# Optimization experiments

Measured on AMD Instinct MI355X. Metric: run time of the kernel, lower is better.

The kernel has to match this reference:

```python
import jax, jax.numpy as jnp
import numpy as np

EPS = 1e-5  # BatchNorm eps


def _spmm(x, src, dst, dinv, n):
    # normalized adjacency SpMM: out[d] = dinv[d] * sum_{(s,d) in E} dinv[s] * x[s]
    msg = x[src] * dinv[src][:, None]                      # [E, d]
    agg = jax.ops.segment_sum(msg, dst, num_segments=n)   # [N, d]
    return agg * dinv[:, None]


def _cheb(x, W, b, src, dst, dinv, n):
    # Chebyshev recursion with lambda_max=2: Lhat = -Ahat
    # T0 = X, T1 = Lhat X, Tk = 2 Lhat T_{k-1} - T_{k-2}; out = sum_k T_k W_k + b
    X0 = x
    X1 = -_spmm(x, src, dst, dinv, n)
    out = X0 @ W[0] + X1 @ W[1]
    Xp, Xc = X0, X1
    for k in range(2, W.shape[0]):
        Xn = -2.0 * _spmm(Xc, src, dst, dinv, n) - Xp
        out = out + Xn @ W[k]
        Xp, Xc = Xc, Xn
    return out + b


def _bn(x, gamma, beta):
    # BatchNorm1d over nodes (training-mode batch stats)
    mu = jnp.mean(x, axis=0)
    var = jnp.var(x, axis=0)
    return (x - mu) * jax.lax.rsqrt(var + EPS) * gamma + beta


def setup_inputs() -> dict:
    key = jax.random.key(0)
    ks = jax.random.split(key, 8)
    n, e, fin, h, fout, K = 50000, 800000, 128, 128, 64, 3
    def w(k, shape, fan_in):
        return jax.random.normal(k, shape, jnp.float32) * np.float32(1.0 / np.sqrt(fan_in))
    return {
        "features": jax.random.normal(ks[0], (n, fin), jnp.float32),
        "src": jax.random.randint(ks[1], (e,), 0, n),
        "dst": jax.random.randint(ks[2], (e,), 0, n),
        "W1": w(ks[3], (K, fin, h), K * fin), "b1": jnp.zeros((h,), jnp.float32),
        "W2": w(ks[4], (K, h, h), K * h), "b2": jnp.zeros((h,), jnp.float32),
        "W3": w(ks[5], (K, h, h), K * h), "b3": jnp.zeros((h,), jnp.float32),
        "gamma": jnp.ones((h,), jnp.float32), "beta": jnp.zeros((h,), jnp.float32),
        "mw1": w(ks[6], (h, h), h), "mb1": jnp.zeros((h,), jnp.float32),
        "mw2": w(ks[7], (h, fout), h), "mb2": jnp.zeros((fout,), jnp.float32),
    }


def reference(features, src, dst, W1, b1, W2, b2, W3, b3, gamma, beta, mw1, mb1, mw2, mb2):
    n = features.shape[0]
    deg = jax.ops.segment_sum(jnp.ones(dst.shape, features.dtype), dst, num_segments=n)
    dinv = jax.lax.rsqrt(jnp.maximum(deg, 1.0))
    x = jax.nn.relu(_cheb(features, W1, b1, src, dst, dinv, n))
    x = _bn(x, gamma, beta)
    for _ in range(1, 3):  # self.k = 3 -> cheb2 applied twice (shared weights)
        x = jax.nn.relu(_cheb(x, W2, b2, src, dst, dinv, n))
    x_res = x
    x = jax.nn.relu(_cheb(x, W3, b3, src, dst, dinv, n))
    x = x + x_res  # dropout treated as identity (eval mode)
    return jax.nn.relu(x @ mw1 + mb1) @ mw2 + mb2
```

## Files before the change

kernel.cpp:

```cpp
#include <hip/hip_runtime.h>
#include <hip/hip_bf16.h>

typedef __attribute__((ext_vector_type(4))) float f32x4;
typedef __attribute__((ext_vector_type(8))) short short8;

__device__ inline unsigned short f2bf(float f) {
    union { float f; unsigned int u; } v; v.f = f;
    unsigned int u = v.u;
    return (unsigned short)((u + 0x7fffu + ((u >> 16) & 1u)) >> 16);
}
__device__ inline float bf2f(unsigned short h) {
    union { unsigned int u; float f; } v; v.u = ((unsigned int)h) << 16; return v.f;
}
__device__ inline float bflo(unsigned int p) {
    union { unsigned int u; float f; } v; v.u = p << 16; return v.f;
}
__device__ inline float bfhi(unsigned int p) {
    union { unsigned int u; float f; } v; v.u = p & 0xffff0000u; return v.f;
}
__device__ inline unsigned int packbf(float a, float b) {
    return (unsigned int)f2bf(a) | ((unsigned int)f2bf(b) << 16);
}

#define EPT 4096


__global__ __launch_bounds__(256) void cast_k(const float* __restrict__ x, unsigned short* __restrict__ y, int n4) {
    int i = blockIdx.x * 256 + threadIdx.x;
    if (i >= n4) return;
    f32x4 v = ((const f32x4*)x)[i];
    uint2 o; o.x = packbf(v[0], v[1]); o.y = packbf(v[2], v[3]);
    ((uint2*)y)[i] = o;
}


__global__ __launch_bounds__(256) void deg_count8_k(const int* __restrict__ dst, int* __restrict__ deg,
                                                    int e, int n, int n8) {
    int r = blockIdx.x & 7;
    int chunk = blockIdx.x >> 3;
    int base = chunk * EPT;
    int lim = base + EPT; if (lim > e) lim = e;
    int lo = r * n8;
    int hi = lo + n8; if (hi > n) hi = n;
    for (int i = base + threadIdx.x; i < lim; i += 256) {
        int d = dst[i];
        if (d >= lo && d < hi) atomicAdd(&deg[d], 1);
    }
}

__global__ __launch_bounds__(256) void partial_k(const int* __restrict__ deg, int* __restrict__ part, int n) {
    __shared__ int sm[256];
    int t = threadIdx.x;
    int base = blockIdx.x * 1024 + t * 4;
    int s = 0;
#pragma unroll
    for (int j = 0; j < 4; ++j) { int idx = base + j; if (idx < n) s += deg[idx]; }
    sm[t] = s;
    __syncthreads();
    for (int off = 128; off > 0; off >>= 1) {
        if (t < off) sm[t] += sm[t + off];
        __syncthreads();
    }
    if (t == 0) part[blockIdx.x] = sm[0];
}

__global__ __launch_bounds__(256) void scanpart_k(int* __restrict__ part, int nb) {
    __shared__ int sm[256];
    int t = threadIdx.x;
    int v = (t < nb) ? part[t] : 0;
    sm[t] = v;
    __syncthreads();
    for (int off = 1; off < 256; off <<= 1) {
        int u = (t >= off) ? sm[t - off] : 0;
        __syncthreads();
        sm[t] += u;
        __syncthreads();
    }
    if (t < nb) part[t] = sm[t] - v;
}

__global__ __launch_bounds__(256) void rowptr_k(const int* __restrict__ deg, const int* __restrict__ part,
                                                int* __restrict__ rowptr, int* __restrict__ cursor,
                                                float* __restrict__ dinv, int n) {
    __shared__ int sm[256];
    int t = threadIdx.x;
    int base = blockIdx.x * 1024 + t * 4;
    int d[4]; int s = 0;
#pragma unroll
    for (int j = 0; j < 4; ++j) { int idx = base + j; d[j] = (idx < n) ? deg[idx] : 0; s += d[j]; }
    sm[t] = s;
    __syncthreads();
    for (int off = 1; off < 256; off <<= 1) {
        int u = (t >= off) ? sm[t - off] : 0;
        __syncthreads();
        sm[t] += u;
        __syncthreads();
    }
    int ex = part[blockIdx.x] + sm[t] - s;
#pragma unroll
    for (int j = 0; j < 4; ++j) {
        int idx = base + j;
        if (idx < n) {
            rowptr[idx] = ex; cursor[idx] = ex;
            dinv[idx] = rsqrtf(fmaxf((float)d[j], 1.0f));
        }
        ex += d[j];
    }
    if (blockIdx.x == gridDim.x - 1 && t == 255) rowptr[n] = part[blockIdx.x] + sm[255];
}

__global__ __launch_bounds__(256) void scatter8_k(const int* __restrict__ src, const int* __restrict__ dst,
                                                  int* __restrict__ cursor, int* __restrict__ csrc,
                                                  int e, int n, int n8) {
    int r = blockIdx.x & 7;
    int chunk = blockIdx.x >> 3;
    int base = chunk * EPT;
    int lim = base + EPT; if (lim > e) lim = e;
    int lo = r * n8;
    int hi = lo + n8; if (hi > n) hi = n;
    for (int i = base + threadIdx.x; i < lim; i += 256) {
        int d = dst[i];
        if (d >= lo && d < hi) {
            int p = atomicAdd(&cursor[d], 1);
            csrc[p] = src[i];
        }
    }
}


template<bool AFF>
__global__ __launch_bounds__(256) void spmm_bf_k(const unsigned short* __restrict__ x, const int* __restrict__ rowptr,
                                                 const int* __restrict__ csrc, const float* __restrict__ dinv,
                                                 const float* __restrict__ gscale, const float* __restrict__ goff,
                                                 unsigned short* __restrict__ out, int n) {
    int lane = threadIdx.x & 63;
    int wave = threadIdx.x >> 6;
    int node = blockIdx.x * 4 + wave;
    if (node >= n) return;
    int g = lane >> 4;
    int c = lane & 15;
    int beg = rowptr[node], end = rowptr[node + 1];
    float acc[8];
    float sw = 0.f;
#pragma unroll
    for (int j = 0; j < 8; ++j) acc[j] = 0.f;

    int i = beg + g;
    for (; i + 12 < end; i += 16) {
        int s0 = csrc[i], s1 = csrc[i + 4], s2 = csrc[i + 8], s3 = csrc[i + 12];
        float w0 = dinv[s0], w1 = dinv[s1], w2 = dinv[s2], w3 = dinv[s3];
        uint4 v0 = ((const uint4*)(x + (size_t)s0 * 128))[c];
        uint4 v1 = ((const uint4*)(x + (size_t)s1 * 128))[c];
        uint4 v2 = ((const uint4*)(x + (size_t)s2 * 128))[c];
        uint4 v3 = ((const uint4*)(x + (size_t)s3 * 128))[c];
        if (AFF) sw += w0 + w1 + w2 + w3;
        acc[0] += w0 * bflo(v0.x); acc[1] += w0 * bfhi(v0.x);
        acc[2] += w0 * bflo(v0.y); acc[3] += w0 * bfhi(v0.y);
        acc[4] += w0 * bflo(v0.z); acc[5] += w0 * bfhi(v0.z);
        acc[6] += w0 * bflo(v0.w); acc[7] += w0 * bfhi(v0.w);
        acc[0] += w1 * bflo(v1.x); acc[1] += w1 * bfhi(v1.x);
        acc[2] += w1 * bflo(v1.y); acc[3] += w1 * bfhi(v1.y);
        acc[4] += w1 * bflo(v1.z); acc[5] += w1 * bfhi(v1.z);
        acc[6] += w1 * bflo(v1.w); acc[7] += w1 * bfhi(v1.w);
        acc[0] += w2 * bflo(v2.x); acc[1] += w2 * bfhi(v2.x);
        acc[2] += w2 * bflo(v2.y); acc[3] += w2 * bfhi(v2.y);
        acc[4] += w2 * bflo(v2.z); acc[5] += w2 * bfhi(v2.z);
        acc[6] += w2 * bflo(v2.w); acc[7] += w2 * bfhi(v2.w);
        acc[0] += w3 * bflo(v3.x); acc[1] += w3 * bfhi(v3.x);
        acc[2] += w3 * bflo(v3.y); acc[3] += w3 * bfhi(v3.y);
        acc[4] += w3 * bflo(v3.z); acc[5] += w3 * bfhi(v3.z);
        acc[6] += w3 * bflo(v3.w); acc[7] += w3 * bfhi(v3.w);
    }
    for (; i < end; i += 4) {
        int s0 = csrc[i];
        float w0 = dinv[s0];
        uint4 v0 = ((const uint4*)(x + (size_t)s0 * 128))[c];
        if (AFF) sw += w0;
        acc[0] += w0 * bflo(v0.x); acc[1] += w0 * bfhi(v0.x);
        acc[2] += w0 * bflo(v0.y); acc[3] += w0 * bfhi(v0.y);
        acc[4] += w0 * bflo(v0.z); acc[5] += w0 * bfhi(v0.z);
        acc[6] += w0 * bflo(v0.w); acc[7] += w0 * bfhi(v0.w);
    }

#pragma unroll
    for (int j = 0; j < 8; ++j) {
        acc[j] += __shfl_xor(acc[j], 16, 64);
        acc[j] += __shfl_xor(acc[j], 32, 64);
    }
    if (AFF) {
        sw += __shfl_xor(sw, 16, 64);
        sw += __shfl_xor(sw, 32, 64);
    }

    float dd = dinv[node];
    if (g == 0) {
        if (AFF) {
            f32x4 sc0 = ((const f32x4*)(gscale + c * 8))[0];
            f32x4 sc1 = ((const f32x4*)(gscale + c * 8))[1];
            f32x4 of0 = ((const f32x4*)(goff + c * 8))[0];
            f32x4 of1 = ((const f32x4*)(goff + c * 8))[1];
#pragma unroll
            for (int j = 0; j < 4; ++j) {
                acc[j] = sc0[j] * acc[j] + of0[j] * sw;
                acc[4 + j] = sc1[j] * acc[4 + j] + of1[j] * sw;
            }
        }
        uint4 o;
        o.x = packbf(acc[0] * dd, acc[1] * dd);
        o.y = packbf(acc[2] * dd, acc[3] * dd);
        o.z = packbf(acc[4] * dd, acc[5] * dd);
        o.w = packbf(acc[6] * dd, acc[7] * dd);
        ((uint4*)(out + (size_t)node * 128))[c] = o;
    }
}


__device__ inline void pack_one(const float* __restrict__ W, unsigned short* __restrict__ out,
                                int K, int N, int cheb, int id) {
    int total = (K / 32) * (N / 16) * 64;
    if (id >= total) return;
    int lane = id & 63;
    int t2 = id >> 6;
    int nf = N / 16;
    int f = t2 % nf;
    int ks = t2 / nf;
    int col = f * 16 + (lane & 15);
    int kbase = ks * 32 + ((lane >> 4) * 8);
    for (int j = 0; j < 8; ++j) {
        int kg = kbase + j;
        float v;
        if (cheb) {
            int t = kg >> 7, kk = kg & 127;
            float w0 = W[kk * 128 + col], wb = W[16384 + kk * 128 + col], wc = W[32768 + kk * 128 + col];
            v = (t == 0) ? (w0 - wc) : (t == 1) ? (-wb) : (2.0f * wc);
        } else {
            v = W[(size_t)kg * N + col];
        }
        out[(size_t)id * 8 + j] = f2bf(v);
    }
}

__global__ __launch_bounds__(256) void pack_all_k(const float* W1, unsigned short* wp1,
                                                  const float* W2, unsigned short* wp2,
                                                  const float* W3, unsigned short* wp3,
                                                  const float* mw1, unsigned short* wpm1,
                                                  const float* mw2, unsigned short* wpm2) {
    int b = blockIdx.x, t = threadIdx.x;
    if (b < 24)       pack_one(W1, wp1, 384, 128, 1, b * 256 + t);
    else if (b < 48)  pack_one(W2, wp2, 384, 128, 1, (b - 24) * 256 + t);
    else if (b < 72)  pack_one(W3, wp3, 384, 128, 1, (b - 48) * 256 + t);
    else if (b < 80)  pack_one(mw1, wpm1, 128, 128, 0, (b - 72) * 256 + t);
    else              pack_one(mw2, wpm2, 128, 64, 0, (b - 80) * 256 + t);
}


__global__ __launch_bounds__(128) void bn_coef_k(const float* __restrict__ gsum, const float* __restrict__ gsqs,
                                                 const float* __restrict__ gamma, const float* __restrict__ beta,
                                                 float* __restrict__ gscale, float* __restrict__ goff, float inv_n) {
    int c = threadIdx.x;
    float mu = gsum[c] * inv_n;
    float var = gsqs[c] * inv_n - mu * mu;
    float sc = rsqrtf(var + 1e-5f) * gamma[c];
    gscale[c] = sc;
    goff[c] = beta[c] - mu * sc;
}


template<bool RELU, bool RES, bool STATS, bool AFFA>
__global__ __launch_bounds__(256, 3) void gemm_k(const unsigned short* __restrict__ s0,
                                                 const unsigned short* __restrict__ s1,
                                                 const unsigned short* __restrict__ s2,
                                                 const unsigned short* __restrict__ wp,
                                                 const float* __restrict__ bias,
                                                 const unsigned short* __restrict__ resid,
                                                 const float* __restrict__ gscale,
                                                 const float* __restrict__ goff,
                                                 float* __restrict__ gsum, float* __restrict__ gsqs,
                                                 unsigned short* __restrict__ outp, int n) {
    __shared__ char blds[49152];
    __shared__ float bs[128], bq[128];
    int t = threadIdx.x;
    int lane = t & 63;
    int wave = t >> 6;
    int row0 = blockIdx.x * 64;

    if (STATS && t < 128) { bs[t] = 0.f; bq[t] = 0.f; }

    int rowA = row0 + wave * 16 + (lane & 15);
    if (rowA >= n) rowA = n - 1;
    int kg = (lane >> 4) * 8;

    {
        const char* gsrc = (const char*)wp;
        int wbase = wave * 12288;
#pragma unroll
        for (int j = 0; j < 12; ++j) {
            int off = wbase + j * 1024;
            __builtin_amdgcn_global_load_lds((const unsigned int*)(gsrc + off + lane * 16),
                                             (unsigned int*)(blds + off), 16, 0, 0);
        }
    }

    short8 a[12];
#pragma unroll
    for (int ks = 0; ks < 12; ++ks) {
        const unsigned short* sp = (ks < 4) ? s0 : ((ks < 8) ? s1 : s2);
        int kk = (ks & 3) * 32 + kg;
        a[ks] = *(const short8*)(sp + (size_t)rowA * 128 + kk);
    }
    if (AFFA) {
#pragma unroll
        for (int ks = 0; ks < 4; ++ks) {
            int kk = ks * 32 + kg;
            union { unsigned short u[8]; short8 v; } af;
#pragma unroll
            for (int j = 0; j < 8; ++j) {
                float xv = bf2f((unsigned short)a[ks][j]);
                af.u[j] = f2bf(xv * gscale[kk + j] + goff[kk + j]);
            }
            a[ks] = af.v;
        }
    }

    f32x4 acc[8];
#pragma unroll
    for (int f = 0; f < 8; ++f) acc[f] = (f32x4)(0.0f);

#pragma unroll
    for (int half = 0; half < 2; ++half) {
        __syncthreads();

#pragma unroll
        for (int ks6 = 0; ks6 < 6; ++ks6) {
            int ks = half * 6 + ks6;
#pragma unroll
            for (int f = 0; f < 8; ++f) {
                short8 bb = *(const short8*)(blds + (ks6 * 8 + f) * 1024 + lane * 16);
                acc[f] = __builtin_amdgcn_mfma_f32_16x16x32_bf16(a[ks], bb, acc[f], 0, 0, 0);
            }
        }

        if (half == 0) {
            __syncthreads();
            const char* gsrc = (const char*)wp + 49152;
            int wbase = wave * 12288;
#pragma unroll
            for (int j = 0; j < 12; ++j) {
                int off = wbase + j * 1024;
                __builtin_amdgcn_global_load_lds((const unsigned int*)(gsrc + off + lane * 16),
                                                 (unsigned int*)(blds + off), 16, 0, 0);
            }
        }
    }

    int colb = lane & 15;
    int rowD = row0 + wave * 16 + ((lane >> 4) << 2);
#pragma unroll
    for (int f = 0; f < 8; ++f) {
        int c = f * 16 + colb;
        float bv = bias[c];
        float ls = 0.f, lq = 0.f;
#pragma unroll
        for (int r = 0; r < 4; ++r) {
            int row = rowD + r;
            if (row >= n) continue;
            float v = acc[f][r] + bv;
            if (RELU) v = fmaxf(v, 0.0f);
            if (RES) v += bf2f(resid[(size_t)row * 128 + c]);
            if (STATS) { ls += v; lq += v * v; }
            outp[(size_t)row * 128 + c] = f2bf(v);
        }
        if (STATS) { atomicAdd(&bs[c], ls); atomicAdd(&bq[c], lq); }
    }

    if (STATS) {
        __syncthreads();
        if (t < 128) {
            atomicAdd(&gsum[t], bs[t]);
            atomicAdd(&gsqs[t], bq[t]);
        }
    }
}


__global__ __launch_bounds__(256, 3) void mlp_fused_k(const unsigned short* __restrict__ x,
                                                      const unsigned short* __restrict__ wpm1,
                                                      const float* __restrict__ mb1,
                                                      const unsigned short* __restrict__ wpm2,
                                                      const float* __restrict__ mb2,
                                                      float* __restrict__ out, int n) {
    __shared__ char alds[49152];
    int t = threadIdx.x;
    int lane = t & 63;
    int wave = t >> 6;
    int row0 = blockIdx.x * 64 + wave * 16;
    int rowA = row0 + (lane & 15);
    if (rowA >= n) rowA = n - 1;
    int kg = (lane >> 4) * 8;
    int colb = lane & 15;

    {
        int wbase = wave * 12288;
#pragma unroll
        for (int j = 0; j < 12; ++j) {
            int off = wbase + j * 1024;
            const char* g = (off < 32768) ? ((const char*)wpm1 + off)
                                          : ((const char*)wpm2 + (off - 32768));
            __builtin_amdgcn_global_load_lds((const unsigned int*)(g + lane * 16),
                                             (unsigned int*)(alds + off), 16, 0, 0);
        }
    }

    short8 a[4];
#pragma unroll
    for (int ks = 0; ks < 4; ++ks)
        a[ks] = *(const short8*)(x + (size_t)rowA * 128 + ks * 32 + kg);

    __syncthreads();

    f32x4 acc[8];
#pragma unroll
    for (int f = 0; f < 8; ++f) acc[f] = (f32x4)(0.0f);
#pragma unroll
    for (int ks = 0; ks < 4; ++ks) {
#pragma unroll
        for (int f = 0; f < 8; ++f) {
            short8 b = *(const short8*)(alds + (ks * 8 + f) * 1024 + lane * 16);
            acc[f] = __builtin_amdgcn_mfma_f32_16x16x32_bf16(a[ks], b, acc[f], 0, 0, 0);
        }
    }
    __syncthreads();

    int lrowD = wave * 16 + ((lane >> 4) << 2);
#pragma unroll
    for (int f = 0; f < 8; ++f) {
        int c = f * 16 + colb;
        float bv = mb1[c];
#pragma unroll
        for (int r = 0; r < 4; ++r) {
            int lrow = lrowD + r;
            float v = fmaxf(acc[f][r] + bv, 0.0f);
            int byte = lrow * 256 + c * 2;
            byte ^= ((lrow & 7) << 4);
            *(unsigned short*)(alds + byte) = f2bf(v);
        }
    }
    __syncthreads();

    f32x4 acc2[4];
#pragma unroll
    for (int f = 0; f < 4; ++f) acc2[f] = (f32x4)(0.0f);
    int lrowA = wave * 16 + (lane & 15);
#pragma unroll
    for (int ks = 0; ks < 4; ++ks) {
        int byte = lrowA * 256 + (ks * 32 + kg) * 2;
        byte ^= ((lrowA & 7) << 4);
        short8 av = *(const short8*)(alds + byte);
#pragma unroll
        for (int f = 0; f < 4; ++f) {
            short8 b = *(const short8*)(alds + 32768 + (ks * 4 + f) * 1024 + lane * 16);
            acc2[f] = __builtin_amdgcn_mfma_f32_16x16x32_bf16(av, b, acc2[f], 0, 0, 0);
        }
    }
    int rowD = row0 + ((lane >> 4) << 2);
#pragma unroll
    for (int f = 0; f < 4; ++f) {
        int c = f * 16 + colb;
        float bv = mb2[c];
#pragma unroll
        for (int r = 0; r < 4; ++r) {
            int row = rowD + r;
            if (row >= n) continue;
            out[(size_t)row * 64 + c] = acc2[f][r] + bv;
        }
    }
}


extern "C" void kernel_launch(void* const* d_in, const int* in_sizes, int n_in,
                              void* d_out, int out_size, void* d_ws, size_t ws_size,
                              hipStream_t stream) {
    const float* feat  = (const float*)d_in[0];
    const int*   src   = (const int*)d_in[1];
    const int*   dst   = (const int*)d_in[2];
    const float* W1    = (const float*)d_in[3];
    const float* b1    = (const float*)d_in[4];
    const float* W2    = (const float*)d_in[5];
    const float* b2    = (const float*)d_in[6];
    const float* W3    = (const float*)d_in[7];
    const float* b3    = (const float*)d_in[8];
    const float* gamma = (const float*)d_in[9];
    const float* beta  = (const float*)d_in[10];
    const float* mw1   = (const float*)d_in[11];
    const float* mb1   = (const float*)d_in[12];
    const float* mw2   = (const float*)d_in[13];
    const float* mb2   = (const float*)d_in[14];
    float* outp = (float*)d_out;

    const int n = in_sizes[0] / 128;
    const int e = in_sizes[1];
    const int n8 = (n + 7) / 8;

    char* w = (char*)d_ws;
    auto alloc = [&](size_t bytes) -> void* {
        void* p = (void*)w;
        w += (bytes + 255) & ~(size_t)255;
        return p;
    };
    unsigned short* featb = (unsigned short*)alloc((size_t)n * 128 * 2);
    unsigned short* buf0  = (unsigned short*)alloc((size_t)n * 128 * 2);
    unsigned short* buf1  = (unsigned short*)alloc((size_t)n * 128 * 2);
    unsigned short* buf2  = (unsigned short*)alloc((size_t)n * 128 * 2);
    unsigned short* buf3  = (unsigned short*)alloc((size_t)n * 128 * 2);
    int*   deg    = (int*)alloc((size_t)n * 4);
    float* dinv   = (float*)alloc((size_t)n * 4);
    int*   rowptr = (int*)alloc((size_t)(n + 1) * 4);
    int*   cursor = (int*)alloc((size_t)n * 4);
    int*   csrc   = (int*)alloc((size_t)e * 4);
    int*   part   = (int*)alloc(256 * 4);
    unsigned short* wp1  = (unsigned short*)alloc(12 * 8 * 512 * 2);
    unsigned short* wp2  = (unsigned short*)alloc(12 * 8 * 512 * 2);
    unsigned short* wp3  = (unsigned short*)alloc(12 * 8 * 512 * 2);
    unsigned short* wpm1 = (unsigned short*)alloc(4 * 8 * 512 * 2);
    unsigned short* wpm2 = (unsigned short*)alloc(4 * 4 * 512 * 2);
    float* gsum   = (float*)alloc(128 * 4);
    float* gsqs   = (float*)alloc(128 * 4);
    float* gscale = (float*)alloc(128 * 4);
    float* goff   = (float*)alloc(128 * 4);

    const int gGemm = (n + 63) / 64;
    const int gSpmm = (n + 3) / 4;
    const int nb = (n + 1023) / 1024;
    const int gE8 = 8 * ((e + EPT - 1) / EPT);

    cast_k<<<(n * 32 + 255) / 256, 256, 0, stream>>>(feat, featb, n * 32);
    hipMemsetAsync(deg, 0, (size_t)n * 4, stream);
    hipMemsetAsync(gsum, 0, 1024, stream);
    deg_count8_k<<<gE8, 256, 0, stream>>>(dst, deg, e, n, n8);
    partial_k<<<nb, 256, 0, stream>>>(deg, part, n);
    scanpart_k<<<1, 256, 0, stream>>>(part, nb);
    rowptr_k<<<nb, 256, 0, stream>>>(deg, part, rowptr, cursor, dinv, n);
    scatter8_k<<<gE8, 256, 0, stream>>>(src, dst, cursor, csrc, e, n, n8);
    pack_all_k<<<84, 256, 0, stream>>>(W1, wp1, W2, wp2, W3, wp3, mw1, wpm1, mw2, wpm2);

    spmm_bf_k<false><<<gSpmm, 256, 0, stream>>>(featb, rowptr, csrc, dinv, nullptr, nullptr, buf1, n);
    spmm_bf_k<false><<<gSpmm, 256, 0, stream>>>(buf1, rowptr, csrc, dinv, nullptr, nullptr, buf2, n);
    gemm_k<true, false, true, false><<<gGemm, 256, 0, stream>>>(
        featb, buf1, buf2, wp1, b1, nullptr, nullptr, nullptr, gsum, gsqs, buf0, n);
    bn_coef_k<<<1, 128, 0, stream>>>(gsum, gsqs, gamma, beta, gscale, goff, 1.0f / (float)n);

    spmm_bf_k<true><<<gSpmm, 256, 0, stream>>>(buf0, rowptr, csrc, dinv, gscale, goff, buf1, n);
    spmm_bf_k<false><<<gSpmm, 256, 0, stream>>>(buf1, rowptr, csrc, dinv, nullptr, nullptr, buf2, n);
    gemm_k<true, false, false, true><<<gGemm, 256, 0, stream>>>(
        buf0, buf1, buf2, wp2, b2, nullptr, gscale, goff, nullptr, nullptr, buf3, n);

    spmm_bf_k<false><<<gSpmm, 256, 0, stream>>>(buf3, rowptr, csrc, dinv, nullptr, nullptr, buf1, n);
    spmm_bf_k<false><<<gSpmm, 256, 0, stream>>>(buf1, rowptr, csrc, dinv, nullptr, nullptr, buf2, n);
    gemm_k<true, false, false, false><<<gGemm, 256, 0, stream>>>(
        buf3, buf1, buf2, wp2, b2, nullptr, nullptr, nullptr, nullptr, nullptr, buf0, n);

    spmm_bf_k<false><<<gSpmm, 256, 0, stream>>>(buf0, rowptr, csrc, dinv, nullptr, nullptr, buf1, n);
    spmm_bf_k<false><<<gSpmm, 256, 0, stream>>>(buf1, rowptr, csrc, dinv, nullptr, nullptr, buf2, n);
    gemm_k<true, true, false, false><<<gGemm, 256, 0, stream>>>(
        buf0, buf1, buf2, wp3, b3, buf0, nullptr, nullptr, nullptr, nullptr, buf3, n);

    mlp_fused_k<<<gGemm, 256, 0, stream>>>(buf3, wpm1, mb1, wpm2, mb2, outp, n);
}
```

Measured before the change: 482.3 us.

## Fuse MLP head into final Chebyshev GEMM and use 512-thread 128-row blocks

The final Chebyshev GEMM now keeps its 128-row output tile in swizzled LDS and runs both MLP layers in place, so the separate MLP kernel and its global round trip of the hidden activations go away. All GEMM launches also move to 512-thread blocks covering 128 rows, so each block loads the packed weights into LDS once for twice as many rows. An empty asm barrier pins the A fragments in registers. The risks are higher LDS use per block (an extra 32KB in the MLP variant) and register pressure under launch_bounds(512,4).

```diff
diff --git a/kernel.cpp b/kernel.cpp
--- a/kernel.cpp
+++ b/kernel.cpp
@@ -266,8 +266,8 @@
 }
 
 
-template<bool RELU, bool RES, bool STATS, bool AFFA>
-__global__ __launch_bounds__(256, 3) void gemm_k(const unsigned short* __restrict__ s0,
+template<bool RELU, bool RES, bool STATS, bool AFFA, bool MLP>
+__global__ __launch_bounds__(512, 4) void gemm_k(const unsigned short* __restrict__ s0,
                                                  const unsigned short* __restrict__ s1,
                                                  const unsigned short* __restrict__ s2,
                                                  const unsigned short* __restrict__ wp,
@@ -276,25 +276,32 @@
                                                  const float* __restrict__ gscale,
                                                  const float* __restrict__ goff,
                                                  float* __restrict__ gsum, float* __restrict__ gsqs,
-                                                 unsigned short* __restrict__ outp, int n) {
+                                                 unsigned short* __restrict__ outp,
+                                                 const unsigned short* __restrict__ wpm1,
+                                                 const float* __restrict__ mb1,
+                                                 const unsigned short* __restrict__ wpm2,
+                                                 const float* __restrict__ mb2,
+                                                 float* __restrict__ outf, int n) {
     __shared__ char blds[49152];
-    __shared__ float bs[128], bq[128];
+    __shared__ char tl[MLP ? 32768 : 16];
+    __shared__ float bs[STATS ? 128 : 1], bq[STATS ? 128 : 1];
     int t = threadIdx.x;
     int lane = t & 63;
     int wave = t >> 6;
-    int row0 = blockIdx.x * 64;
+    int row0 = blockIdx.x * 128;
 
     if (STATS && t < 128) { bs[t] = 0.f; bq[t] = 0.f; }
 
     int rowA = row0 + wave * 16 + (lane & 15);
     if (rowA >= n) rowA = n - 1;
     int kg = (lane >> 4) * 8;
+    int colb = lane & 15;
 
     {
         const char* gsrc = (const char*)wp;
-        int wbase = wave * 12288;
-#pragma unroll
-        for (int j = 0; j < 12; ++j) {
+        int wbase = wave * 6144;
+#pragma unroll
+        for (int j = 0; j < 6; ++j) {
             int off = wbase + j * 1024;
             __builtin_amdgcn_global_load_lds((const unsigned int*)(gsrc + off + lane * 16),
                                              (unsigned int*)(blds + off), 16, 0, 0);
@@ -321,6 +328,11 @@
             a[ks] = af.v;
         }
     }
+#pragma unroll
+    for (int ks = 0; ks < 12; ++ks) {
+        f32x4 kv = *(f32x4*)&a[ks];
+        asm volatile("" :: "v"(kv));
+    }
 
     f32x4 acc[8];
 #pragma unroll
@@ -343,9 +355,9 @@
         if (half == 0) {
             __syncthreads();
             const char* gsrc = (const char*)wp + 49152;
-            int wbase = wave * 12288;
-#pragma unroll
-            for (int j = 0; j < 12; ++j) {
+            int wbase = wave * 6144;
+#pragma unroll
+            for (int j = 0; j < 6; ++j) {
                 int off = wbase + j * 1024;
                 __builtin_amdgcn_global_load_lds((const unsigned int*)(gsrc + off + lane * 16),
                                                  (unsigned int*)(blds + off), 16, 0, 0);
@@ -353,8 +365,8 @@
         }
     }
 
-    int colb = lane & 15;
     int rowD = row0 + wave * 16 + ((lane >> 4) << 2);
+    int lrowD = wave * 16 + ((lane >> 4) << 2);
 #pragma unroll
     for (int f = 0; f < 8; ++f) {
         int c = f * 16 + colb;
@@ -368,7 +380,14 @@
             if (RELU) v = fmaxf(v, 0.0f);
             if (RES) v += bf2f(resid[(size_t)row * 128 + c]);
             if (STATS) { ls += v; lq += v * v; }
-            outp[(size_t)row * 128 + c] = f2bf(v);
+            if (MLP) {
+                int lrow = lrowD + r;
+                int byte = lrow * 256 + c * 2;
+                byte ^= ((lrow & 7) << 4);
+                *(unsigned short*)(tl + byte) = f2bf(v);
+            } else {
+                outp[(size_t)row * 128 + c] = f2bf(v);
+            }
         }
         if (STATS) { atomicAdd(&bs[c], ls); atomicAdd(&bq[c], lq); }
     }
@@ -380,98 +399,78 @@
             atomicAdd(&gsqs[t], bq[t]);
         }
     }
-}
-
-
-__global__ __launch_bounds__(256, 3) void mlp_fused_k(const unsigned short* __restrict__ x,
-                                                      const unsigned short* __restrict__ wpm1,
-                                                      const float* __restrict__ mb1,
-                                                      const unsigned short* __restrict__ wpm2,
-                                                      const float* __restrict__ mb2,
-                                                      float* __restrict__ out, int n) {
-    __shared__ char alds[49152];
-    int t = threadIdx.x;
-    int lane = t & 63;
-    int wave = t >> 6;
-    int row0 = blockIdx.x * 64 + wave * 16;
-    int rowA = row0 + (lane & 15);
-    if (rowA >= n) rowA = n - 1;
-    int kg = (lane >> 4) * 8;
-    int colb = lane & 15;
-
-    {
-        int wbase = wave * 12288;
-#pragma unroll
-        for (int j = 0; j < 12; ++j) {
-            int off = wbase + j * 1024;
-            const char* g = (off < 32768) ? ((const char*)wpm1 + off)
-                                          : ((const char*)wpm2 + (off - 32768));
-            __builtin_amdgcn_global_load_lds((const unsigned int*)(g + lane * 16),
-                                             (unsigned int*)(alds + off), 16, 0, 0);
-        }
-    }
-
-    short8 a[4];
-#pragma unroll
-    for (int ks = 0; ks < 4; ++ks)
-        a[ks] = *(const short8*)(x + (size_t)rowA * 128 + ks * 32 + kg);
-
-    __syncthreads();
-
-    f32x4 acc[8];
-#pragma unroll
-    for (int f = 0; f < 8; ++f) acc[f] = (f32x4)(0.0f);
-#pragma unroll
-    for (int ks = 0; ks < 4; ++ks) {
+
+    if (MLP) {
+        __syncthreads();
+        {
+            int wbase = wave * 6144;
+#pragma unroll
+            for (int j = 0; j < 6; ++j) {
+                int off = wbase + j * 1024;
+                const char* g = (off < 32768) ? ((const char*)wpm1 + off)
+                                              : ((const char*)wpm2 + (off - 32768));
+                __builtin_amdgcn_global_load_lds((const unsigned int*)(g + lane * 16),
+                                                 (unsigned int*)(blds + off), 16, 0, 0);
+            }
+        }
+        __syncthreads();
+
+        int lrowA = wave * 16 + (lane & 15);
+        f32x4 acc2[8];
+#pragma unroll
+        for (int f = 0; f < 8; ++f) acc2[f] = (f32x4)(0.0f);
+#pragma unroll
+        for (int ks = 0; ks < 4; ++ks) {
+            int byte = lrowA * 256 + (ks * 32 + kg) * 2;
+            byte ^= ((lrowA & 7) << 4);
+            short8 av = *(const short8*)(tl + byte);
+#pragma unroll
+            for (int f = 0; f < 8; ++f) {
+                short8 b = *(const short8*)(blds + (ks * 8 + f) * 1024 + lane * 16);
+                acc2[f] = __builtin_amdgcn_mfma_f32_16x16x32_bf16(av, b, acc2[f], 0, 0, 0);
+            }
+        }
+        __syncthreads();
+
 #pragma unroll
         for (int f = 0; f < 8; ++f) {
-            short8 b = *(const short8*)(alds + (ks * 8 + f) * 1024 + lane * 16);
-            acc[f] = __builtin_amdgcn_mfma_f32_16x16x32_bf16(a[ks], b, acc[f], 0, 0, 0);
-        }
-    }
-    __syncthreads();
-
-    int lrowD = wave * 16 + ((lane >> 4) << 2);
-#pragma unroll
-    for (int f = 0; f < 8; ++f) {
-        int c = f * 16 + colb;
-        float bv = mb1[c];
-#pragma unroll
-        for (int r = 0; r < 4; ++r) {
-            int lrow = lrowD + r;
-            float v = fmaxf(acc[f][r] + bv, 0.0f);
-            int byte = lrow * 256 + c * 2;
-            byte ^= ((lrow & 7) << 4);
-            *(unsigned short*)(alds + byte) = f2bf(v);
-        }
-    }
-    __syncthreads();
-
-    f32x4 acc2[4];
-#pragma unroll
-    for (int f = 0; f < 4; ++f) acc2[f] = (f32x4)(0.0f);
-    int lrowA = wave * 16 + (lane & 15);
-#pragma unroll
-    for (int ks = 0; ks < 4; ++ks) {
-        int byte = lrowA * 256 + (ks * 32 + kg) * 2;
-        byte ^= ((lrowA & 7) << 4);
-        short8 av = *(const short8*)(alds + byte);
+            int c = f * 16 + colb;
+            float bv = mb1[c];
+#pragma unroll
+            for (int r = 0; r < 4; ++r) {
+                int lrow = lrowD + r;
+                float v = fmaxf(acc2[f][r] + bv, 0.0f);
+                int byte = lrow * 256 + c * 2;
+                byte ^= ((lrow & 7) << 4);
+                *(unsigned short*)(tl + byte) = f2bf(v);
+            }
+        }
+        __syncthreads();
+
+        f32x4 acc3[4];
+#pragma unroll
+        for (int f = 0; f < 4; ++f) acc3[f] = (f32x4)(0.0f);
+#pragma unroll
+        for (int ks = 0; ks < 4; ++ks) {
+            int byte = lrowA * 256 + (ks * 32 + kg) * 2;
+            byte ^= ((lrowA & 7) << 4);
+            short8 av = *(const short8*)(tl + byte);
+#pragma unroll
+            for (int f = 0; f < 4; ++f) {
+                short8 b = *(const short8*)(blds + 32768 + (ks * 4 + f) * 1024 + lane * 16);
+                acc3[f] = __builtin_amdgcn_mfma_f32_16x16x32_bf16(av, b, acc3[f], 0, 0, 0);
+            }
+        }
 #pragma unroll
         for (int f = 0; f < 4; ++f) {
-            short8 b = *(const short8*)(alds + 32768 + (ks * 4 + f) * 1024 + lane * 16);
-            acc2[f] = __builtin_amdgcn_mfma_f32_16x16x32_bf16(av, b, acc2[f], 0, 0, 0);
-        }
-    }
-    int rowD = row0 + ((lane >> 4) << 2);
-#pragma unroll
-    for (int f = 0; f < 4; ++f) {
-        int c = f * 16 + colb;
-        float bv = mb2[c];
-#pragma unroll
-        for (int r = 0; r < 4; ++r) {
-            int row = rowD + r;
-            if (row >= n) continue;
-            out[(size_t)row * 64 + c] = acc2[f][r] + bv;
+            int c = f * 16 + colb;
+            float bv = mb2[c];
+#pragma unroll
+            for (int r = 0; r < 4; ++r) {
+                int row = rowD + r;
+                if (row >= n) continue;
+                outf[(size_t)row * 64 + c] = acc3[f][r] + bv;
+            }
         }
     }
 }
@@ -528,7 +527,7 @@
     float* gscale = (float*)alloc(128 * 4);
     float* goff   = (float*)alloc(128 * 4);
 
-    const int gGemm = (n + 63) / 64;
+    const int gGemm = (n + 127) / 128;
     const int gSpmm = (n + 3) / 4;
     const int nb = (n + 1023) / 1024;
     const int gE8 = 8 * ((e + EPT - 1) / EPT);
@@ -545,24 +544,26 @@
 
     spmm_bf_k<false><<<gSpmm, 256, 0, stream>>>(featb, rowptr, csrc, dinv, nullptr, nullptr, buf1, n);
     spmm_bf_k<false><<<gSpmm, 256, 0, stream>>>(buf1, rowptr, csrc, dinv, nullptr, nullptr, buf2, n);
-    gemm_k<true, false, true, false><<<gGemm, 256, 0, stream>>>(
-        featb, buf1, buf2, wp1, b1, nullptr, nullptr, nullptr, gsum, gsqs, buf0, n);
+    gemm_k<true, false, true, false, false><<<gGemm, 512, 0, stream>>>(
+        featb, buf1, buf2, wp1, b1, nullptr, nullptr, nullptr, gsum, gsqs, buf0,
+        nullptr, nullptr, nullptr, nullptr, nullptr, n);
     bn_coef_k<<<1, 128, 0, stream>>>(gsum, gsqs, gamma, beta, gscale, goff, 1.0f / (float)n);
 
     spmm_bf_k<true><<<gSpmm, 256, 0, stream>>>(buf0, rowptr, csrc, dinv, gscale, goff, buf1, n);
     spmm_bf_k<false><<<gSpmm, 256, 0, stream>>>(buf1, rowptr, csrc, dinv, nullptr, nullptr, buf2, n);
-    gemm_k<true, false, false, true><<<gGemm, 256, 0, stream>>>(
-        buf0, buf1, buf2, wp2, b2, nullptr, gscale, goff, nullptr, nullptr, buf3, n);
+    gemm_k<true, false, false, true, false><<<gGemm, 512, 0, stream>>>(
+        buf0, buf1, buf2, wp2, b2, nullptr, gscale, goff, nullptr, nullptr, buf3,
+        nullptr, nullptr, nullptr, nullptr, nullptr, n);
 
     spmm_bf_k<false><<<gSpmm, 256, 0, stream>>>(buf3, rowptr, csrc, dinv, nullptr, nullptr, buf1, n);
     spmm_bf_k<false><<<gSpmm, 256, 0, stream>>>(buf1, rowptr, csrc, dinv, nullptr, nullptr, buf2, n);
-    gemm_k<true, false, false, false><<<gGemm, 256, 0, stream>>>(
-        buf3, buf1, buf2, wp2, b2, nullptr, nullptr, nullptr, nullptr, nullptr, buf0, n);
+    gemm_k<true, false, false, false, false><<<gGemm, 512, 0, stream>>>(
+        buf3, buf1, buf2, wp2, b2, nullptr, nullptr, nullptr, nullptr, nullptr, buf0,
+        nullptr, nullptr, nullptr, nullptr, nullptr, n);
 
     spmm_bf_k<false><<<gSpmm, 256, 0, stream>>>(buf0, rowptr, csrc, dinv, nullptr, nullptr, buf1, n);
     spmm_bf_k<false><<<gSpmm, 256, 0, stream>>>(buf1, rowptr, csrc, dinv, nullptr, nullptr, buf2, n);
-    gemm_k<true, true, false, false><<<gGemm, 256, 0, stream>>>(
-        buf0, buf1, buf2, wp3, b3, buf0, nullptr, nullptr, nullptr, nullptr, buf3, n);
-
-    mlp_fused_k<<<gGemm, 256, 0, stream>>>(buf3, wpm1, mb1, wpm2, mb2, outp, n);
-}
+    gemm_k<true, true, false, false, true><<<gGemm, 512, 0, stream>>>(
+        buf0, buf1, buf2, wp3, b3, buf0, nullptr, nullptr, nullptr, nullptr, nullptr,
+        wpm1, mb1, wpm2, mb2, outp, n);
+}
```

Result: faster. 455.7 us (-5.5%).
